# Kernel tuning notes

Hardware: AMD Instinct MI355X
Metric: run time of the kernel (lower is better)

## Reference

```python
import jax, jax.numpy as jnp
import numpy as np

N_PRO, N_WAT, E = 60000, 40000, 1000000
N = N_PRO + N_WAT
IN_DIM, HID, HEADS = 21, 32, 4
EDGE_K, EDGE_DIM = 32, 32
RADIUS_MAX = 5.0
FF_HID, OUT_DIM = 128, 2
HC = HID * HEADS


def setup_inputs() -> dict:
    key = jax.random.key(0)
    ks = jax.random.split(key, 32)

    def glorot(k, shape):
        fan = shape[0] + shape[-1]
        return jax.random.normal(k, shape, jnp.float32) * jnp.sqrt(2.0 / fan)

    inp = {
        'protein_pos': jax.random.normal(ks[0], (N_PRO, 3), jnp.float32),
        'water_pos': jax.random.normal(ks[1], (N_WAT, 3), jnp.float32),
        'protein_features': jax.random.uniform(ks[2], (N_PRO, IN_DIM), jnp.float32),
        'edge_index': jax.random.randint(ks[3], (2, E), 0, N, jnp.int64),
        'gamma': jnp.array([10.0], jnp.float32),
        # feature_emb
        'Wf': glorot(ks[4], (IN_DIM, HID)), 'bf': jnp.zeros((HID,), jnp.float32),
        # edge_emb
        'We': glorot(ks[5], (EDGE_K, EDGE_DIM)), 'be': jnp.zeros((EDGE_DIM,), jnp.float32),
        # conv1 (in: HID)
        'W1': glorot(ks[6], (HID, HC)),
        'att_src1': glorot(ks[7], (HEADS, HID)), 'att_dst1': glorot(ks[8], (HEADS, HID)),
        'Wedge1': glorot(ks[9], (EDGE_DIM, HC)), 'att_edge1': glorot(ks[10], (HEADS, HID)),
        'b1': jnp.zeros((HC,), jnp.float32),
        # conv2 (in: HC)
        'W2': glorot(ks[11], (HC, HC)),
        'att_src2': glorot(ks[12], (HEADS, HID)), 'att_dst2': glorot(ks[13], (HEADS, HID)),
        'Wedge2': glorot(ks[14], (EDGE_DIM, HC)), 'att_edge2': glorot(ks[15], (HEADS, HID)),
        'b2': jnp.zeros((HC,), jnp.float32),
        # mlp
        'Wm1': glorot(ks[16], (HC, FF_HID)), 'bm1': jnp.zeros((FF_HID,), jnp.float32),
        'Wm2': glorot(ks[17], (FF_HID, OUT_DIM)), 'bm2': jnp.zeros((OUT_DIM,), jnp.float32),
    }
    return inp


def gat_conv(h, edge_attr, src, dst, W, att_s, att_d, Wedge, att_e, b):
    # h: [N, Din] -> x: [N, H, C]; edge features only modulate attention logits.
    x = (h @ W).reshape(N, HEADS, HID)
    e = (edge_attr @ Wedge).reshape(-1, HEADS, HID)
    a_s = jnp.einsum('nhc,hc->nh', x, att_s)   # [N,H]
    a_d = jnp.einsum('nhc,hc->nh', x, att_d)   # [N,H]
    a_e = jnp.einsum('ehc,hc->eh', e, att_e)   # [E,H]
    alpha = jax.nn.leaky_relu(a_s[src] + a_d[dst] + a_e, 0.2)  # [E,H]
    # segment softmax over incoming edges of each dst node
    m = jax.ops.segment_max(alpha, dst, num_segments=N)
    m = jnp.where(jnp.isfinite(m), m, 0.0)
    ex = jnp.exp(alpha - m[dst])
    den = jax.ops.segment_sum(ex, dst, num_segments=N)
    coef = ex / (den[dst] + 1e-16)             # [E,H]
    msg = x[src] * coef[:, :, None]            # [E,H,C]
    out = jax.ops.segment_sum(msg, dst, num_segments=N)  # [N,H,C]
    return out.reshape(N, HC) + b


def reference(protein_pos, water_pos, protein_features, edge_index, gamma,
              Wf, bf, We, be,
              W1, att_src1, att_dst1, Wedge1, att_edge1, b1,
              W2, att_src2, att_dst2, Wedge2, att_edge2, b2,
              Wm1, bm1, Wm2, bm2):
    pos = jnp.concatenate([protein_pos, water_pos], axis=0)  # [N,3]
    src, dst = edge_index[0], edge_index[1]
    edge_vec = pos[dst] - pos[src]
    edge_dis = jnp.linalg.norm(edge_vec, axis=-1)            # [E]
    # RBF expansion of distances
    centers = jnp.linspace(0.0, RADIUS_MAX, EDGE_K)
    edge_h = jnp.exp(-gamma[0] * (edge_dis[:, None] - centers[None, :]) ** 2)  # [E,K]
    edge_attr = edge_h @ We + be                             # [E,EDGE_DIM]

    # water nodes get one-hot 'water' feature in last slot
    water_feat = jnp.zeros((N_WAT, IN_DIM), protein_features.dtype).at[:, -1].set(1.0)
    feats = jnp.concatenate([protein_features, water_feat], axis=0)
    h = feats @ Wf + bf                                      # [N,HID]

    h = jax.nn.elu(gat_conv(h, edge_attr, src, dst, W1, att_src1, att_dst1, Wedge1, att_edge1, b1))
    h = jax.nn.elu(gat_conv(h, edge_attr, src, dst, W2, att_src2, att_dst2, Wedge2, att_edge2, b2))

    h = jax.nn.relu(h @ Wm1 + bm1) @ Wm2 + bm2               # [N,OUT_DIM]
    return h[N_PRO:]                                         # water nodes only
```

## Files before the change

kernel.cpp:

```cpp
#include <hip/hip_runtime.h>
#include <hip/hip_fp16.h>
#include <stdint.h>

#define N_PRO 60000
#define N_WAT 40000
#define NN    100000
#define NNP   100032
#define NE    1000000
#define IN_DIM 21
#define HID    32
#define HEADS  4
#define HC     128
#define EDGE_K 32
#define LUTN   2048
#define NH0B  ((NNP * 32) / 256)
#define NBUCK 196
#define EPT   8
#define SCATB ((NE / EPT + 255) / 256)
#define FCAP  6144

typedef _Float16 half8 __attribute__((ext_vector_type(8)));
typedef float    f32x4 __attribute__((ext_vector_type(4)));

__global__ __launch_bounds__(256) void k_small(
    const float* We, const float* be,
    const float* Wedge1, const float* atte1,
    const float* Wedge2, const float* atte2,
    const float* Wf, const float* bfv,
    const float* W1, const float* atts1, const float* attd1,
    float* smallw)
{
    __shared__ float V[2][128];
    int t = threadIdx.x;
    {
        int l = t >> 7, dh = t & 127, d = dh >> 2, h = dh & 3;
        const float* Wg = l ? Wedge2 : Wedge1;
        const float* ae = l ? atte2 : atte1;
        float s = 0.f;
        for (int c = 0; c < HID; c++)
            s += Wg[d * HC + h * HID + c] * ae[h * HID + c];
        V[l][dh] = s;
    }
    __syncthreads();
    {
        int l = t >> 7, kh = t & 127, k = kh >> 2, h = kh & 3;
        float s = 0.f;
        for (int d = 0; d < 32; d++)
            s += We[k * 32 + d] * V[l][d * 4 + h];
        smallw[(l ? 132 : 0) + kh] = s;
    }
    if (t < 8) {
        int l = t >> 2, h = t & 3;
        float s = 0.f;
        for (int d = 0; d < 32; d++)
            s += be[d] * V[l][d * 4 + h];
        smallw[(l ? 260 : 128) + h] = s;
    }
    if (t >= 32 && t < 64) {
        int c = t - 32;
        smallw[264 + c] = Wf[20 * 32 + c] + bfv[c];
    }
    {
        int side = t >> 7;
        int h = (t >> 5) & 3, c = t & 31;
        const float* av = side ? attd1 : atts1;
        float s = 0.f;
        for (int j = 0; j < 32; j++)
            s += W1[c * 128 + h * 32 + j] * av[h * 32 + j];
        smallw[(side ? 424 : 296) + (t & 127)] = s;
    }
}

__global__ __launch_bounds__(256) void k_lut(
    const float* __restrict__ smallw, const float* __restrict__ gamma,
    float* __restrict__ lut)
{
    int e = blockIdx.x * 256 + threadIdx.x;
    if (e >= 2 * LUTN) return;
    int layer = e >> 11, bin = e & (LUTN - 1);
    const float* U = smallw + (layer ? 132 : 0);
    const float* aeb = smallw + (layer ? 260 : 128);
    float dd = bin * (1.0f / 256.0f);
    float g = gamma[0];
    float a0 = aeb[0], a1 = aeb[1], a2 = aeb[2], a3 = aeb[3];
    const float step = 5.0f / 31.0f;
    #pragma unroll
    for (int k = 0; k < EDGE_K; k++) {
        float tt = dd - (float)k * step;
        float r = __expf(-g * tt * tt);
        a0 += r * U[k * 4 + 0];
        a1 += r * U[k * 4 + 1];
        a2 += r * U[k * 4 + 2];
        a3 += r * U[k * 4 + 3];
    }
    *(float4*)&lut[(size_t)e * 4] = make_float4(a0, a1, a2, a3);
}

__global__ __launch_bounds__(256) void k_h0(
    const float* __restrict__ pf, const float* __restrict__ Wf,
    const float* __restrict__ bfv, const float* __restrict__ smallw,
    __half* __restrict__ h0, float* __restrict__ asd)
{
    int t = threadIdx.x;
    __shared__ float Wfs[IN_DIM * 32];
    __shared__ float bfs[32];
    __shared__ float h0w[32];
    __shared__ float vas[128], vad[128];
    for (int i = t; i < IN_DIM * 32; i += 256) Wfs[i] = Wf[i];
    if (t < 32) { bfs[t] = bfv[t]; h0w[t] = smallw[264 + t]; }
    if (t < 128) vas[t] = smallw[296 + t];
    else         vad[t - 128] = smallw[424 + (t - 128)];
    __syncthreads();
    int id = blockIdx.x * 256 + t;
    int n = id >> 5, c = id & 31;
    if (n >= NNP) return;
    float v;
    if (n < N_PRO) {
        float s = bfs[c];
        for (int k = 0; k < IN_DIM; k++)
            s += pf[n * IN_DIM + k] * Wfs[k * 32 + c];
        v = s;
    } else {
        v = h0w[c];
    }
    h0[(size_t)n * 32 + c] = __float2half(v);
    float ps[4], pd[4];
    #pragma unroll
    for (int h = 0; h < 4; h++) {
        ps[h] = v * vas[h * 32 + c];
        pd[h] = v * vad[h * 32 + c];
    }
    #pragma unroll
    for (int m = 1; m < 32; m <<= 1) {
        #pragma unroll
        for (int h = 0; h < 4; h++) {
            ps[h] += __shfl_xor(ps[h], m, 64);
            pd[h] += __shfl_xor(pd[h], m, 64);
        }
    }
    if ((t & 31) == 0) {
        *(float4*)&asd[(size_t)n * 8]     = make_float4(ps[0], ps[1], ps[2], ps[3]);
        *(float4*)&asd[(size_t)n * 8 + 4] = make_float4(pd[0], pd[1], pd[2], pd[3]);
    }
}

__global__ __launch_bounds__(256) void k_bcnt(
    const int* __restrict__ ei, int* __restrict__ gbh)
{
    __shared__ int lh[256];
    int t = threadIdx.x;
    lh[t] = 0;
    __syncthreads();
    int e0 = (blockIdx.x * 256 + t) * EPT;
    if (e0 < NE) {
        int4 da = *(const int4*)&ei[NE + e0];
        int4 db = *(const int4*)&ei[NE + e0 + 4];
        int ds[8] = {da.x, da.y, da.z, da.w, db.x, db.y, db.z, db.w};
        #pragma unroll
        for (int j = 0; j < EPT; j++)
            if ((unsigned)ds[j] < (unsigned)NN)
                atomicAdd(&lh[ds[j] >> 9], 1);
    }
    __syncthreads();
    if (t < NBUCK && lh[t]) atomicAdd(&gbh[t], lh[t]);
}

__global__ __launch_bounds__(256) void k_bscan(
    const int* __restrict__ gbh, int* __restrict__ gboff,
    int* __restrict__ gcur, int* __restrict__ offp)
{
    __shared__ int s[256];
    int t = threadIdx.x;
    int v = (t < NBUCK) ? gbh[t] : 0;
    s[t] = v;
    __syncthreads();
    #pragma unroll
    for (int o = 1; o < 256; o <<= 1) {
        int x = (t >= o) ? s[t - o] : 0;
        __syncthreads();
        s[t] += x;
        __syncthreads();
    }
    int ex = s[t] - v;
    if (t < NBUCK) { gboff[t] = ex; gcur[t] = ex; }
    if (t == NBUCK - 1) { gboff[NBUCK] = s[t]; offp[NN] = s[t]; }
}

__global__ __launch_bounds__(256) void k_scat(
    const int* __restrict__ ei, const float* __restrict__ ppos,
    const float* __restrict__ wpos, int* __restrict__ gcur,
    uint2* __restrict__ ebuf2)
{
    __shared__ int lh[256];
    __shared__ int lbase[256];
    int t = threadIdx.x;
    lh[t] = 0;
    __syncthreads();
    int e0 = (blockIdx.x * 256 + t) * EPT;
    int bkt[EPT], rnk[EPT];
    unsigned rec0[EPT], rec1[EPT];
    #pragma unroll
    for (int j = 0; j < EPT; j++) bkt[j] = -1;
    if (e0 < NE) {
        int4 sa = *(const int4*)&ei[e0];
        int4 sb = *(const int4*)&ei[e0 + 4];
        int4 da = *(const int4*)&ei[NE + e0];
        int4 db = *(const int4*)&ei[NE + e0 + 4];
        int ss[8] = {sa.x, sa.y, sa.z, sa.w, sb.x, sb.y, sb.z, sb.w};
        int ds[8] = {da.x, da.y, da.z, da.w, db.x, db.y, db.z, db.w};
        #pragma unroll
        for (int j = 0; j < EPT; j++) {
            int s = ss[j], d = ds[j];
            if ((unsigned)d < (unsigned)NN) {
                const float* ps = (s < N_PRO) ? &ppos[s * 3] : &wpos[(s - N_PRO) * 3];
                const float* pd = (d < N_PRO) ? &ppos[d * 3] : &wpos[(d - N_PRO) * 3];
                float dx = pd[0] - ps[0];
                float dy = pd[1] - ps[1];
                float dz = pd[2] - ps[2];
                float dist = sqrtf(dx * dx + dy * dy + dz * dz);
                unsigned code = (unsigned)fminf(dist * 4096.0f, 32767.0f);
                bkt[j] = d >> 9;
                rec0[j] = ((unsigned)d << 15) | code;
                rec1[j] = (unsigned)s;
                rnk[j] = atomicAdd(&lh[bkt[j]], 1);
            }
        }
    }
    __syncthreads();
    if (t < NBUCK) lbase[t] = lh[t] ? atomicAdd(&gcur[t], lh[t]) : 0;
    __syncthreads();
    #pragma unroll
    for (int j = 0; j < EPT; j++)
        if (bkt[j] >= 0)
            ebuf2[lbase[bkt[j]] + rnk[j]] = make_uint2(rec0[j], rec1[j]);
}

__global__ __launch_bounds__(1024) void k_fine(
    const int* __restrict__ gboff, const uint2* __restrict__ ebuf2,
    const float* __restrict__ lutg, const float* __restrict__ asd,
    int* __restrict__ offp, unsigned* __restrict__ e4,
    float* __restrict__ wb)
{
    __shared__ uint2 eL[FCAP];
    __shared__ int lcnt[512], lexc[512], ssc[512];
    int b = blockIdx.x, t = threadIdx.x;
    int beg = gboff[b];
    int nb = gboff[b + 1] - beg;
    bool inl = (nb <= FCAP);
    if (inl)
        for (int i = t; i < nb; i += 1024) eL[i] = ebuf2[beg + i];
    if (t < 512) lcnt[t] = 0;
    __syncthreads();
    for (int i = t; i < nb; i += 1024) {
        uint2 u = inl ? eL[i] : ebuf2[beg + i];
        atomicAdd(&lcnt[(u.x >> 15) & 511], 1);
    }
    __syncthreads();
    int c = (t < 512) ? lcnt[t] : 0;
    if (t < 512) ssc[t] = c;
    __syncthreads();
    for (int o = 1; o < 512; o <<= 1) {
        int x = (t >= o && t < 512) ? ssc[t - o] : 0;
        __syncthreads();
        if (t < 512) ssc[t] += x;
        __syncthreads();
    }
    if (t < 512) {
        lexc[t] = ssc[t] - c;
        int node = b * 512 + t;
        if (node < NN) offp[node] = beg + lexc[t];
        lcnt[t] = 0;
    }
    __syncthreads();
    for (int i = t; i < nb; i += 1024) {
        uint2 u = inl ? eL[i] : ebuf2[beg + i];
        int ln = (int)((u.x >> 15) & 511u);
        int r = atomicAdd(&lcnt[ln], 1);
        int p = beg + lexc[ln] + r;
        unsigned code = u.x & 32767u;
        unsigned s = u.y;
        e4[p] = (s << 15) | code;
        int n = (b << 9) + ln;
        float f = fminf((float)code * 0.0625f, (float)(LUTN - 2));
        int i0 = (int)f;
        float fr = f - (float)i0;
        float4 A = *(const float4*)&lutg[(size_t)i0 * 4];
        float4 B = *(const float4*)&lutg[(size_t)(i0 + 1) * 4];
        float4 as4 = *(const float4*)&asd[(size_t)s * 8];
        float4 ad4 = *(const float4*)&asd[(size_t)n * 8 + 4];
        float v0 = as4.x + ad4.x + A.x + (B.x - A.x) * fr;
        float v1 = as4.y + ad4.y + A.y + (B.y - A.y) * fr;
        float v2 = as4.z + ad4.z + A.z + (B.z - A.z) * fr;
        float v3 = as4.w + ad4.w + A.w + (B.w - A.w) * fr;
        v0 = fmaxf(v0, 0.2f * v0);
        v1 = fmaxf(v1, 0.2f * v1);
        v2 = fmaxf(v2, 0.2f * v2);
        v3 = fmaxf(v3, 0.2f * v3);
        *(float4*)&wb[(size_t)p * 4] = make_float4(
            __expf(v0), __expf(v1), __expf(v2), __expf(v3));
    }
}

__global__ __launch_bounds__(256) void k_xm(
    const __half* __restrict__ h, const float* __restrict__ Wg,
    const float* __restrict__ atts, const float* __restrict__ attd,
    __half* __restrict__ x16, float* __restrict__ asd)
{
    __shared__ __half Wt[128 * 136];
    __shared__ float attS[128], attD[128];
    int t = threadIdx.x;
    for (int i = t; i < 128 * 32; i += 256) {
        int c = i & 127, d = (i >> 7) * 4;
        float w0 = Wg[(d + 0) * 128 + c];
        float w1 = Wg[(d + 1) * 128 + c];
        float w2 = Wg[(d + 2) * 128 + c];
        float w3 = Wg[(d + 3) * 128 + c];
        __half2 p0 = __floats2half2_rn(w0, w1);
        __half2 p1 = __floats2half2_rn(w2, w3);
        uint2 pk;
        pk.x = *(unsigned*)&p0;
        pk.y = *(unsigned*)&p1;
        *(uint2*)&Wt[c * 136 + d] = pk;
    }
    if (t < 128) { attS[t] = atts[t]; attD[t] = attd[t]; }
    __syncthreads();
    int wv = t >> 6, lane = t & 63;
    int m16 = lane & 15, quad = lane >> 4;
    int n0 = blockIdx.x * 64 + wv * 16;
    f32x4 acc[8];
    #pragma unroll
    for (int ct = 0; ct < 8; ct++) acc[ct] = (f32x4){0.f, 0.f, 0.f, 0.f};
    #pragma unroll
    for (int ks = 0; ks < 4; ks++) {
        int d0 = ks * 32 + quad * 8;
        half8 bf = *(const half8*)&h[(size_t)(n0 + m16) * 128 + d0];
        #pragma unroll
        for (int ct = 0; ct < 8; ct++) {
            half8 af = *(const half8*)&Wt[(ct * 16 + m16) * 136 + d0];
            acc[ct] = __builtin_amdgcn_mfma_f32_16x16x32_f16(af, bf, acc[ct], 0, 0, 0);
        }
    }
    __half* xrow = &x16[(size_t)(n0 + m16) * 128 + quad * 4];
    float ps[4] = {0.f, 0.f, 0.f, 0.f}, pd[4] = {0.f, 0.f, 0.f, 0.f};
    #pragma unroll
    for (int ct = 0; ct < 8; ct++) {
        f32x4 a = acc[ct];
        __half2 h0p = __floats2half2_rn(a[0], a[1]);
        __half2 h1p = __floats2half2_rn(a[2], a[3]);
        uint2 pk;
        pk.x = *(unsigned*)&h0p;
        pk.y = *(unsigned*)&h1p;
        *(uint2*)&xrow[ct * 16] = pk;
        int cb = ct * 16 + quad * 4;
        int hh = ct >> 1;
        ps[hh] += a[0] * attS[cb] + a[1] * attS[cb + 1]
                + a[2] * attS[cb + 2] + a[3] * attS[cb + 3];
        pd[hh] += a[0] * attD[cb] + a[1] * attD[cb + 1]
                + a[2] * attD[cb + 2] + a[3] * attD[cb + 3];
    }
    #pragma unroll
    for (int hh = 0; hh < 4; hh++) {
        ps[hh] += __shfl_xor(ps[hh], 16, 64);
        ps[hh] += __shfl_xor(ps[hh], 32, 64);
        pd[hh] += __shfl_xor(pd[hh], 16, 64);
        pd[hh] += __shfl_xor(pd[hh], 32, 64);
    }
    if (lane < 16) {
        int n = n0 + m16;
        *(float4*)&asd[(size_t)n * 8]     = make_float4(ps[0], ps[1], ps[2], ps[3]);
        *(float4*)&asd[(size_t)n * 8 + 4] = make_float4(pd[0], pd[1], pd[2], pd[3]);
    }
}

__global__ __launch_bounds__(256) void k_w2(
    const int* __restrict__ off, const unsigned* __restrict__ e4,
    const float* __restrict__ lutg, const float* __restrict__ asd,
    float* __restrict__ wb)
{
    int wv = threadIdx.x >> 6, lane = threadIdx.x & 63;
    int n = N_PRO + blockIdx.x * 4 + wv;
    if (n >= NN) return;
    int beg = off[n], end = off[n + 1];
    float4 ad4 = *(const float4*)&asd[(size_t)n * 8 + 4];
    for (int i = beg + lane; i < end; i += 64) {
        unsigned u = e4[i];
        unsigned s = u >> 15;
        float f = fminf((float)(u & 32767u) * 0.0625f, (float)(LUTN - 2));
        int i0 = (int)f;
        float fr = f - (float)i0;
        float4 A = *(const float4*)&lutg[(size_t)i0 * 4];
        float4 B = *(const float4*)&lutg[(size_t)(i0 + 1) * 4];
        float4 as4 = *(const float4*)&asd[(size_t)s * 8];
        float v0 = as4.x + ad4.x + A.x + (B.x - A.x) * fr;
        float v1 = as4.y + ad4.y + A.y + (B.y - A.y) * fr;
        float v2 = as4.z + ad4.z + A.z + (B.z - A.z) * fr;
        float v3 = as4.w + ad4.w + A.w + (B.w - A.w) * fr;
        v0 = fmaxf(v0, 0.2f * v0);
        v1 = fmaxf(v1, 0.2f * v1);
        v2 = fmaxf(v2, 0.2f * v2);
        v3 = fmaxf(v3, 0.2f * v3);
        *(float4*)&wb[(size_t)i * 4] = make_float4(
            __expf(v0), __expf(v1), __expf(v2), __expf(v3));
    }
}

__global__ __launch_bounds__(256) void k_aggz(
    const int* __restrict__ off, const unsigned* __restrict__ e4,
    const float* __restrict__ wb, const __half* __restrict__ h016,
    __half* __restrict__ zbuf)
{
    int t = threadIdx.x;
    int wv = t >> 6, lane = t & 63;
    int g = lane >> 4, q = lane & 15;
    int n = blockIdx.x * 16 + wv * 4 + g;
    int beg = off[n], end = off[n + 1];
    const __half2* x2 = (const __half2*)h016;
    float a0x = 0.f, a0y = 0.f, a1x = 0.f, a1y = 0.f;
    float a2x = 0.f, a2y = 0.f, a3x = 0.f, a3y = 0.f;
    float l0 = 0.f, l1 = 0.f, l2 = 0.f, l3 = 0.f;
    int i = beg;
    for (; i + 1 < end; i += 2) {
        unsigned u0 = e4[i], u1 = e4[i + 1];
        float4 w0 = *(const float4*)&wb[(size_t)i * 4];
        float4 w1 = *(const float4*)&wb[(size_t)(i + 1) * 4];
        float2 x0 = __half22float2(x2[(u0 >> 15) * 16u + q]);
        float2 x1 = __half22float2(x2[(u1 >> 15) * 16u + q]);
        a0x += w0.x * x0.x + w1.x * x1.x;  a0y += w0.x * x0.y + w1.x * x1.y;
        a1x += w0.y * x0.x + w1.y * x1.x;  a1y += w0.y * x0.y + w1.y * x1.y;
        a2x += w0.z * x0.x + w1.z * x1.x;  a2y += w0.z * x0.y + w1.z * x1.y;
        a3x += w0.w * x0.x + w1.w * x1.x;  a3y += w0.w * x0.y + w1.w * x1.y;
        l0 += w0.x + w1.x;  l1 += w0.y + w1.y;
        l2 += w0.z + w1.z;  l3 += w0.w + w1.w;
    }
    if (i < end) {
        unsigned u0 = e4[i];
        float4 w0 = *(const float4*)&wb[(size_t)i * 4];
        float2 x0 = __half22float2(x2[(u0 >> 15) * 16u + q]);
        a0x += w0.x * x0.x;  a0y += w0.x * x0.y;
        a1x += w0.y * x0.x;  a1y += w0.y * x0.y;
        a2x += w0.z * x0.x;  a2y += w0.z * x0.y;
        a3x += w0.w * x0.x;  a3y += w0.w * x0.y;
        l0 += w0.x; l1 += w0.y; l2 += w0.z; l3 += w0.w;
    }
    float i0v = 1.0f / (l0 + 1e-16f);
    float i1v = 1.0f / (l1 + 1e-16f);
    float i2v = 1.0f / (l2 + 1e-16f);
    float i3v = 1.0f / (l3 + 1e-16f);
    __half* zr = &zbuf[(size_t)n * 128];
    *(__half2*)&zr[      q * 2] = __floats2half2_rn(a0x * i0v, a0y * i0v);
    *(__half2*)&zr[32  + q * 2] = __floats2half2_rn(a1x * i1v, a1y * i1v);
    *(__half2*)&zr[64  + q * 2] = __floats2half2_rn(a2x * i2v, a2y * i2v);
    *(__half2*)&zr[96  + q * 2] = __floats2half2_rn(a3x * i3v, a3y * i3v);
}

__global__ __launch_bounds__(256) void k_zm(
    const __half* __restrict__ zbuf, const float* __restrict__ W1g,
    const float* __restrict__ b1, __half* __restrict__ hbuf)
{
    __shared__ __half Wt[128 * 40];
    int t = threadIdx.x;
    for (int i = t; i < 128 * 8; i += 256) {
        int c = i & 127, k4 = (i >> 7) * 4;
        float w0 = W1g[(k4 + 0) * 128 + c];
        float w1 = W1g[(k4 + 1) * 128 + c];
        float w2 = W1g[(k4 + 2) * 128 + c];
        float w3 = W1g[(k4 + 3) * 128 + c];
        __half2 p0 = __floats2half2_rn(w0, w1);
        __half2 p1 = __floats2half2_rn(w2, w3);
        uint2 pk;
        pk.x = *(unsigned*)&p0;
        pk.y = *(unsigned*)&p1;
        *(uint2*)&Wt[c * 40 + k4] = pk;
    }
    __syncthreads();
    int wv = t >> 6, lane = t & 63;
    int m16 = lane & 15, quad = lane >> 4;
    int n0 = blockIdx.x * 64 + wv * 16;
    half8 bf[4];
    #pragma unroll
    for (int hh = 0; hh < 4; hh++)
        bf[hh] = *(const half8*)&zbuf[(size_t)(n0 + m16) * 128 + hh * 32 + quad * 8];
    f32x4 acc[8];
    #pragma unroll
    for (int ct = 0; ct < 8; ct++) {
        half8 af = *(const half8*)&Wt[(ct * 16 + m16) * 40 + quad * 8];
        acc[ct] = __builtin_amdgcn_mfma_f32_16x16x32_f16(
            af, bf[ct >> 1], (f32x4){0.f, 0.f, 0.f, 0.f}, 0, 0, 0);
    }
    __half* orow = &hbuf[(size_t)(n0 + m16) * 128 + quad * 4];
    #pragma unroll
    for (int ct = 0; ct < 8; ct++) {
        int cb = ct * 16 + quad * 4;
        float4 bb = *(const float4*)&b1[cb];
        float r0 = acc[ct][0] + bb.x;
        float r1 = acc[ct][1] + bb.y;
        float r2 = acc[ct][2] + bb.z;
        float r3 = acc[ct][3] + bb.w;
        r0 = r0 > 0.f ? r0 : __expf(r0) - 1.0f;
        r1 = r1 > 0.f ? r1 : __expf(r1) - 1.0f;
        r2 = r2 > 0.f ? r2 : __expf(r2) - 1.0f;
        r3 = r3 > 0.f ? r3 : __expf(r3) - 1.0f;
        __half2 ha = __floats2half2_rn(r0, r1);
        __half2 hb = __floats2half2_rn(r2, r3);
        uint2 pk;
        pk.x = *(unsigned*)&ha;
        pk.y = *(unsigned*)&hb;
        *(uint2*)&orow[ct * 16] = pk;
    }
}

__global__ __launch_bounds__(256) void k_agg2(
    const int* __restrict__ off, const unsigned* __restrict__ e4,
    const float* __restrict__ wb, const __half* __restrict__ x16,
    const float* __restrict__ bias, __half* __restrict__ hout)
{
    int t = threadIdx.x;
    int wv = t >> 6, lane = t & 63;
    int g = lane >> 5, q = lane & 31;
    int n = N_PRO + blockIdx.x * 8 + wv * 2 + g;
    int h = q >> 3;
    int beg = off[n], end = off[n + 1];
    float ax = 0.f, ay = 0.f, az = 0.f, aw = 0.f, ls = 0.f;
    int i = beg;
    for (; i + 1 < end; i += 2) {
        unsigned u0 = e4[i], u1 = e4[i + 1];
        float w0 = wb[(size_t)i * 4 + h];
        float w1 = wb[(size_t)(i + 1) * 4 + h];
        float2 r0 = *(const float2*)&x16[(size_t)(u0 >> 15) * 128 + q * 4];
        float2 r1 = *(const float2*)&x16[(size_t)(u1 >> 15) * 128 + q * 4];
        float2 f00 = __half22float2(*(__half2*)&r0.x);
        float2 f01 = __half22float2(*(__half2*)&r0.y);
        float2 f10 = __half22float2(*(__half2*)&r1.x);
        float2 f11 = __half22float2(*(__half2*)&r1.y);
        ax += w0 * f00.x + w1 * f10.x;
        ay += w0 * f00.y + w1 * f10.y;
        az += w0 * f01.x + w1 * f11.x;
        aw += w0 * f01.y + w1 * f11.y;
        ls += w0 + w1;
    }
    if (i < end) {
        unsigned u0 = e4[i];
        float w0 = wb[(size_t)i * 4 + h];
        float2 r0 = *(const float2*)&x16[(size_t)(u0 >> 15) * 128 + q * 4];
        float2 f00 = __half22float2(*(__half2*)&r0.x);
        float2 f01 = __half22float2(*(__half2*)&r0.y);
        ax += w0 * f00.x; ay += w0 * f00.y;
        az += w0 * f01.x; aw += w0 * f01.y;
        ls += w0;
    }
    float inv = 1.0f / (ls + 1e-16f);
    float4 bb = *(const float4*)&bias[q * 4];
    float o0 = ax * inv + bb.x;
    float o1 = ay * inv + bb.y;
    float o2 = az * inv + bb.z;
    float o3 = aw * inv + bb.w;
    o0 = o0 > 0.f ? o0 : __expf(o0) - 1.0f;
    o1 = o1 > 0.f ? o1 : __expf(o1) - 1.0f;
    o2 = o2 > 0.f ? o2 : __expf(o2) - 1.0f;
    o3 = o3 > 0.f ? o3 : __expf(o3) - 1.0f;
    __half2 ha = __floats2half2_rn(o0, o1);
    __half2 hb = __floats2half2_rn(o2, o3);
    uint2 pk;
    pk.x = *(unsigned*)&ha;
    pk.y = *(unsigned*)&hb;
    *(uint2*)&hout[(size_t)n * 128 + q * 4] = pk;
}

__global__ __launch_bounds__(256) void k_mlp(
    const __half* __restrict__ hh, const float* __restrict__ Wm1,
    const float* __restrict__ bm1, const float* __restrict__ Wm2,
    const float* __restrict__ bm2, float* __restrict__ out)
{
    __shared__ __half Wt[128 * 136];
    __shared__ float b1s[128];
    __shared__ float w2s[256];
    int t = threadIdx.x;
    for (int i = t; i < 128 * 32; i += 256) {
        int c = i & 127, d = (i >> 7) * 4;
        float w0 = Wm1[(d + 0) * 128 + c];
        float w1 = Wm1[(d + 1) * 128 + c];
        float w2 = Wm1[(d + 2) * 128 + c];
        float w3 = Wm1[(d + 3) * 128 + c];
        __half2 p0 = __floats2half2_rn(w0, w1);
        __half2 p1 = __floats2half2_rn(w2, w3);
        uint2 pk;
        pk.x = *(unsigned*)&p0;
        pk.y = *(unsigned*)&p1;
        *(uint2*)&Wt[c * 136 + d] = pk;
    }
    if (t < 128) b1s[t] = bm1[t];
    w2s[t] = Wm2[t];
    __syncthreads();
    int wv = t >> 6, lane = t & 63;
    int m16 = lane & 15, quad = lane >> 4;
    int n0 = blockIdx.x * 64 + wv * 16;
    f32x4 acc[8];
    #pragma unroll
    for (int ct = 0; ct < 8; ct++) acc[ct] = (f32x4){0.f, 0.f, 0.f, 0.f};
    #pragma unroll
    for (int ks = 0; ks < 4; ks++) {
        int d0 = ks * 32 + quad * 8;
        half8 bf = *(const half8*)&hh[(size_t)(N_PRO + n0 + m16) * 128 + d0];
        #pragma unroll
        for (int ct = 0; ct < 8; ct++) {
            half8 af = *(const half8*)&Wt[(ct * 16 + m16) * 136 + d0];
            acc[ct] = __builtin_amdgcn_mfma_f32_16x16x32_f16(af, bf, acc[ct], 0, 0, 0);
        }
    }
    float p0 = 0.f, p1 = 0.f;
    #pragma unroll
    for (int ct = 0; ct < 8; ct++) {
        int cb = ct * 16 + quad * 4;
        float4 bb = *(const float4*)&b1s[cb];
        float r0 = fmaxf(acc[ct][0] + bb.x, 0.f);
        float r1 = fmaxf(acc[ct][1] + bb.y, 0.f);
        float r2 = fmaxf(acc[ct][2] + bb.z, 0.f);
        float r3 = fmaxf(acc[ct][3] + bb.w, 0.f);
        p0 += r0 * w2s[(cb + 0) * 2] + r1 * w2s[(cb + 1) * 2]
            + r2 * w2s[(cb + 2) * 2] + r3 * w2s[(cb + 3) * 2];
        p1 += r0 * w2s[(cb + 0) * 2 + 1] + r1 * w2s[(cb + 1) * 2 + 1]
            + r2 * w2s[(cb + 2) * 2 + 1] + r3 * w2s[(cb + 3) * 2 + 1];
    }
    p0 += __shfl_xor(p0, 16, 64);
    p0 += __shfl_xor(p0, 32, 64);
    p1 += __shfl_xor(p1, 16, 64);
    p1 += __shfl_xor(p1, 32, 64);
    if (lane < 16) {
        int wn = n0 + m16;
        *(float2*)&out[(size_t)wn * 2] = make_float2(p0 + bm2[0], p1 + bm2[1]);
    }
}

extern "C" void kernel_launch(void* const* d_in, const int* in_sizes, int n_in,
                              void* d_out, int out_size, void* d_ws, size_t ws_size,
                              hipStream_t stream)
{
    const float* ppos   = (const float*)d_in[0];
    const float* wpos   = (const float*)d_in[1];
    const float* pfeat  = (const float*)d_in[2];
    const int*   ei     = (const int*)d_in[3];
    const float* gamma  = (const float*)d_in[4];
    const float* Wf     = (const float*)d_in[5];
    const float* bfv    = (const float*)d_in[6];
    const float* We     = (const float*)d_in[7];
    const float* be     = (const float*)d_in[8];
    const float* W1     = (const float*)d_in[9];
    const float* atts1  = (const float*)d_in[10];
    const float* attd1  = (const float*)d_in[11];
    const float* Wedge1 = (const float*)d_in[12];
    const float* atte1  = (const float*)d_in[13];
    const float* b1     = (const float*)d_in[14];
    const float* W2     = (const float*)d_in[15];
    const float* atts2  = (const float*)d_in[16];
    const float* attd2  = (const float*)d_in[17];
    const float* Wedge2 = (const float*)d_in[18];
    const float* atte2  = (const float*)d_in[19];
    const float* b2     = (const float*)d_in[20];
    const float* Wm1    = (const float*)d_in[21];
    const float* bm1    = (const float*)d_in[22];
    const float* Wm2    = (const float*)d_in[23];
    const float* bm2    = (const float*)d_in[24];
    float* out = (float*)d_out;

    char* ws = (char*)d_ws;
    size_t o = 0;
    auto alloc = [&](size_t bytes) -> char* {
        char* p = ws + o;
        o += (bytes + 255) & ~(size_t)255;
        return p;
    };
    __half*   h0      = (__half*)alloc((size_t)NNP * 32 * 2);
    __half*   x16     = (__half*)alloc((size_t)NNP * 128 * 2);
    __half*   hbuf    = (__half*)alloc((size_t)NNP * 128 * 2);
    float*    asd     = (float*)alloc((size_t)NNP * 8 * 4);
    float*    wb      = (float*)alloc((size_t)NE * 4 * 4);
    int*      offp    = (int*)alloc((size_t)(NN + 1) * 4);
    unsigned* e4      = (unsigned*)alloc((size_t)NE * 4);
    int*      gbh     = (int*)alloc(256 * 4);
    int*      gboff   = (int*)alloc(256 * 4);
    int*      gcur    = (int*)alloc(256 * 4);
    float*    smallw  = (float*)alloc(4096);
    float*    lutbuf  = (float*)alloc((size_t)2 * LUTN * 4 * 4);
    uint2*    ebuf2   = (uint2*)hbuf;

    hipMemsetAsync(gbh, 0, 256 * 4, stream);
    k_small<<<1, 256, 0, stream>>>(We, be, Wedge1, atte1, Wedge2, atte2, Wf, bfv,
                                   W1, atts1, attd1, smallw);
    k_lut<<<(2 * LUTN + 255) / 256, 256, 0, stream>>>(smallw, gamma, lutbuf);
    k_h0<<<NH0B, 256, 0, stream>>>(pfeat, Wf, bfv, smallw, h0, asd);
    k_bcnt<<<SCATB, 256, 0, stream>>>(ei, gbh);
    k_bscan<<<1, 256, 0, stream>>>(gbh, gboff, gcur, offp);
    k_scat<<<SCATB, 256, 0, stream>>>(ei, ppos, wpos, gcur, ebuf2);
    k_fine<<<NBUCK, 1024, 0, stream>>>(gboff, ebuf2, lutbuf, asd, offp, e4, wb);
    k_aggz<<<NN / 16, 256, 0, stream>>>(offp, e4, wb, h0, x16);
    k_zm<<<NNP / 64, 256, 0, stream>>>(x16, W1, b1, hbuf);
    k_xm<<<NNP / 64, 256, 0, stream>>>(hbuf, W2, atts2, attd2, x16, asd);
    k_w2<<<N_WAT / 4, 256, 0, stream>>>(offp, e4, lutbuf + (size_t)LUTN * 4, asd, wb);
    k_agg2<<<N_WAT / 8, 256, 0, stream>>>(offp, e4, wb, x16, b2, hbuf);
    k_mlp<<<N_WAT / 64, 256, 0, stream>>>(hbuf, Wm1, bm1, Wm2, bm2, out);
}
```

Measured before the change: 325.3 us.

## Fuse bucket count into h0, fuse conv2 weights into aggregation, faster scans

Merges the bucket-histogram kernel into k_h0 as extra blocks, so one launch covers both and they can run concurrently. Removes k_w2 and computes the conv2 attention weights inline in k_agg2 from the LUT and asd, which drops the write and reread of wb. Replaces the shared-memory Hillis-Steele scan in k_fine with a wave-level shuffle scan plus a small cross-wave scan, and unrolls the k_aggz edge loop by 4 for more memory-level parallelism. In exchange, k_agg2 recomputes each edge weight in every one of the 8 lanes that share a head, and the merged k_h0 now has two divergent block types.

After: 310.5 us. -4.6%, faster.

```diff
diff --git a/kernel.cpp b/kernel.cpp
--- a/kernel.cpp
+++ b/kernel.cpp
@@ -99,9 +99,28 @@
 __global__ __launch_bounds__(256) void k_h0(
     const float* __restrict__ pf, const float* __restrict__ Wf,
     const float* __restrict__ bfv, const float* __restrict__ smallw,
+    const int* __restrict__ ei, int* __restrict__ gbh,
     __half* __restrict__ h0, float* __restrict__ asd)
 {
     int t = threadIdx.x;
+    if (blockIdx.x >= NH0B) {
+        __shared__ int lh[256];
+        lh[t] = 0;
+        __syncthreads();
+        int e0 = ((blockIdx.x - NH0B) * 256 + t) * EPT;
+        if (e0 < NE) {
+            int4 da = *(const int4*)&ei[NE + e0];
+            int4 db = *(const int4*)&ei[NE + e0 + 4];
+            int ds[8] = {da.x, da.y, da.z, da.w, db.x, db.y, db.z, db.w};
+            #pragma unroll
+            for (int j = 0; j < EPT; j++)
+                if ((unsigned)ds[j] < (unsigned)NN)
+                    atomicAdd(&lh[ds[j] >> 9], 1);
+        }
+        __syncthreads();
+        if (t < NBUCK && lh[t]) atomicAdd(&gbh[t], lh[t]);
+        return;
+    }
     __shared__ float Wfs[IN_DIM * 32];
     __shared__ float bfs[32];
     __shared__ float h0w[32];
@@ -142,27 +161,6 @@
         *(float4*)&asd[(size_t)n * 8]     = make_float4(ps[0], ps[1], ps[2], ps[3]);
         *(float4*)&asd[(size_t)n * 8 + 4] = make_float4(pd[0], pd[1], pd[2], pd[3]);
     }
-}
-
-__global__ __launch_bounds__(256) void k_bcnt(
-    const int* __restrict__ ei, int* __restrict__ gbh)
-{
-    __shared__ int lh[256];
-    int t = threadIdx.x;
-    lh[t] = 0;
-    __syncthreads();
-    int e0 = (blockIdx.x * 256 + t) * EPT;
-    if (e0 < NE) {
-        int4 da = *(const int4*)&ei[NE + e0];
-        int4 db = *(const int4*)&ei[NE + e0 + 4];
-        int ds[8] = {da.x, da.y, da.z, da.w, db.x, db.y, db.z, db.w};
-        #pragma unroll
-        for (int j = 0; j < EPT; j++)
-            if ((unsigned)ds[j] < (unsigned)NN)
-                atomicAdd(&lh[ds[j] >> 9], 1);
-    }
-    __syncthreads();
-    if (t < NBUCK && lh[t]) atomicAdd(&gbh[t], lh[t]);
 }
 
 __global__ __launch_bounds__(256) void k_bscan(
@@ -242,7 +240,8 @@
     float* __restrict__ wb)
 {
     __shared__ uint2 eL[FCAP];
-    __shared__ int lcnt[512], lexc[512], ssc[512];
+    __shared__ int lcnt[512], lexc[512];
+    __shared__ int wsum[8];
     int b = blockIdx.x, t = threadIdx.x;
     int beg = gboff[b];
     int nb = gboff[b + 1] - beg;
@@ -256,17 +255,32 @@
         atomicAdd(&lcnt[(u.x >> 15) & 511], 1);
     }
     __syncthreads();
-    int c = (t < 512) ? lcnt[t] : 0;
-    if (t < 512) ssc[t] = c;
-    __syncthreads();
-    for (int o = 1; o < 512; o <<= 1) {
-        int x = (t >= o && t < 512) ? ssc[t - o] : 0;
-        __syncthreads();
-        if (t < 512) ssc[t] += x;
-        __syncthreads();
-    }
     if (t < 512) {
-        lexc[t] = ssc[t] - c;
+        int c = lcnt[t];
+        int lane = t & 63;
+        int v = c;
+        #pragma unroll
+        for (int d = 1; d < 64; d <<= 1) {
+            int x = __shfl_up(v, d, 64);
+            if (lane >= d) v += x;
+        }
+        if (lane == 63) wsum[t >> 6] = v;
+        lexc[t] = v - c;
+    }
+    __syncthreads();
+    if (t < 8) {
+        int orig = wsum[t];
+        int v = orig;
+        #pragma unroll
+        for (int d = 1; d < 8; d <<= 1) {
+            int x = __shfl_up(v, d, 64);
+            if (t >= d) v += x;
+        }
+        wsum[t] = v - orig;
+    }
+    __syncthreads();
+    if (t < 512) {
+        lexc[t] += wsum[t >> 6];
         int node = b * 512 + t;
         if (node < NN) offp[node] = beg + lexc[t];
         lcnt[t] = 0;
@@ -372,38 +386,6 @@
     }
 }
 
-__global__ __launch_bounds__(256) void k_w2(
-    const int* __restrict__ off, const unsigned* __restrict__ e4,
-    const float* __restrict__ lutg, const float* __restrict__ asd,
-    float* __restrict__ wb)
-{
-    int wv = threadIdx.x >> 6, lane = threadIdx.x & 63;
-    int n = N_PRO + blockIdx.x * 4 + wv;
-    if (n >= NN) return;
-    int beg = off[n], end = off[n + 1];
-    float4 ad4 = *(const float4*)&asd[(size_t)n * 8 + 4];
-    for (int i = beg + lane; i < end; i += 64) {
-        unsigned u = e4[i];
-        unsigned s = u >> 15;
-        float f = fminf((float)(u & 32767u) * 0.0625f, (float)(LUTN - 2));
-        int i0 = (int)f;
-        float fr = f - (float)i0;
-        float4 A = *(const float4*)&lutg[(size_t)i0 * 4];
-        float4 B = *(const float4*)&lutg[(size_t)(i0 + 1) * 4];
-        float4 as4 = *(const float4*)&asd[(size_t)s * 8];
-        float v0 = as4.x + ad4.x + A.x + (B.x - A.x) * fr;
-        float v1 = as4.y + ad4.y + A.y + (B.y - A.y) * fr;
-        float v2 = as4.z + ad4.z + A.z + (B.z - A.z) * fr;
-        float v3 = as4.w + ad4.w + A.w + (B.w - A.w) * fr;
-        v0 = fmaxf(v0, 0.2f * v0);
-        v1 = fmaxf(v1, 0.2f * v1);
-        v2 = fmaxf(v2, 0.2f * v2);
-        v3 = fmaxf(v3, 0.2f * v3);
-        *(float4*)&wb[(size_t)i * 4] = make_float4(
-            __expf(v0), __expf(v1), __expf(v2), __expf(v3));
-    }
-}
-
 __global__ __launch_bounds__(256) void k_aggz(
     const int* __restrict__ off, const unsigned* __restrict__ e4,
     const float* __restrict__ wb, const __half* __restrict__ h016,
@@ -419,20 +401,31 @@
     float a2x = 0.f, a2y = 0.f, a3x = 0.f, a3y = 0.f;
     float l0 = 0.f, l1 = 0.f, l2 = 0.f, l3 = 0.f;
     int i = beg;
-    for (; i + 1 < end; i += 2) {
-        unsigned u0 = e4[i], u1 = e4[i + 1];
+    for (; i + 3 < end; i += 4) {
+        unsigned u0 = e4[i],     u1 = e4[i + 1];
+        unsigned u2 = e4[i + 2], u3 = e4[i + 3];
         float4 w0 = *(const float4*)&wb[(size_t)i * 4];
         float4 w1 = *(const float4*)&wb[(size_t)(i + 1) * 4];
+        float4 w2 = *(const float4*)&wb[(size_t)(i + 2) * 4];
+        float4 w3 = *(const float4*)&wb[(size_t)(i + 3) * 4];
         float2 x0 = __half22float2(x2[(u0 >> 15) * 16u + q]);
         float2 x1 = __half22float2(x2[(u1 >> 15) * 16u + q]);
-        a0x += w0.x * x0.x + w1.x * x1.x;  a0y += w0.x * x0.y + w1.x * x1.y;
-        a1x += w0.y * x0.x + w1.y * x1.x;  a1y += w0.y * x0.y + w1.y * x1.y;
-        a2x += w0.z * x0.x + w1.z * x1.x;  a2y += w0.z * x0.y + w1.z * x1.y;
-        a3x += w0.w * x0.x + w1.w * x1.x;  a3y += w0.w * x0.y + w1.w * x1.y;
-        l0 += w0.x + w1.x;  l1 += w0.y + w1.y;
-        l2 += w0.z + w1.z;  l3 += w0.w + w1.w;
-    }
-    if (i < end) {
+        float2 x2v = __half22float2(x2[(u2 >> 15) * 16u + q]);
+        float2 x3 = __half22float2(x2[(u3 >> 15) * 16u + q]);
+        a0x += w0.x * x0.x + w1.x * x1.x + w2.x * x2v.x + w3.x * x3.x;
+        a0y += w0.x * x0.y + w1.x * x1.y + w2.x * x2v.y + w3.x * x3.y;
+        a1x += w0.y * x0.x + w1.y * x1.x + w2.y * x2v.x + w3.y * x3.x;
+        a1y += w0.y * x0.y + w1.y * x1.y + w2.y * x2v.y + w3.y * x3.y;
+        a2x += w0.z * x0.x + w1.z * x1.x + w2.z * x2v.x + w3.z * x3.x;
+        a2y += w0.z * x0.y + w1.z * x1.y + w2.z * x2v.y + w3.z * x3.y;
+        a3x += w0.w * x0.x + w1.w * x1.x + w2.w * x2v.x + w3.w * x3.x;
+        a3y += w0.w * x0.y + w1.w * x1.y + w2.w * x2v.y + w3.w * x3.y;
+        l0 += (w0.x + w1.x) + (w2.x + w3.x);
+        l1 += (w0.y + w1.y) + (w2.y + w3.y);
+        l2 += (w0.z + w1.z) + (w2.z + w3.z);
+        l3 += (w0.w + w1.w) + (w2.w + w3.w);
+    }
+    for (; i < end; i++) {
         unsigned u0 = e4[i];
         float4 w0 = *(const float4*)&wb[(size_t)i * 4];
         float2 x0 = __half22float2(x2[(u0 >> 15) * 16u + q]);
@@ -511,8 +504,9 @@
 
 __global__ __launch_bounds__(256) void k_agg2(
     const int* __restrict__ off, const unsigned* __restrict__ e4,
-    const float* __restrict__ wb, const __half* __restrict__ x16,
-    const float* __restrict__ bias, __half* __restrict__ hout)
+    const float* __restrict__ lutg, const float* __restrict__ asd,
+    const __half* __restrict__ x16, const float* __restrict__ bias,
+    __half* __restrict__ hout)
 {
     int t = threadIdx.x;
     int wv = t >> 6, lane = t & 63;
@@ -520,14 +514,26 @@
     int n = N_PRO + blockIdx.x * 8 + wv * 2 + g;
     int h = q >> 3;
     int beg = off[n], end = off[n + 1];
+    float adh = asd[(size_t)n * 8 + 4 + h];
     float ax = 0.f, ay = 0.f, az = 0.f, aw = 0.f, ls = 0.f;
     int i = beg;
     for (; i + 1 < end; i += 2) {
         unsigned u0 = e4[i], u1 = e4[i + 1];
-        float w0 = wb[(size_t)i * 4 + h];
-        float w1 = wb[(size_t)(i + 1) * 4 + h];
-        float2 r0 = *(const float2*)&x16[(size_t)(u0 >> 15) * 128 + q * 4];
-        float2 r1 = *(const float2*)&x16[(size_t)(u1 >> 15) * 128 + q * 4];
+        unsigned s0 = u0 >> 15, s1 = u1 >> 15;
+        float f0 = fminf((float)(u0 & 32767u) * 0.0625f, (float)(LUTN - 2));
+        float f1 = fminf((float)(u1 & 32767u) * 0.0625f, (float)(LUTN - 2));
+        int i00 = (int)f0, i10 = (int)f1;
+        float fr0 = f0 - (float)i00, fr1 = f1 - (float)i10;
+        float A0 = lutg[i00 * 4 + h], B0 = lutg[(i00 + 1) * 4 + h];
+        float A1 = lutg[i10 * 4 + h], B1 = lutg[(i10 + 1) * 4 + h];
+        float as0 = asd[(size_t)s0 * 8 + h], as1 = asd[(size_t)s1 * 8 + h];
+        float2 r0 = *(const float2*)&x16[(size_t)s0 * 128 + q * 4];
+        float2 r1 = *(const float2*)&x16[(size_t)s1 * 128 + q * 4];
+        float v0 = as0 + adh + A0 + (B0 - A0) * fr0;
+        float v1 = as1 + adh + A1 + (B1 - A1) * fr1;
+        v0 = fmaxf(v0, 0.2f * v0);
+        v1 = fmaxf(v1, 0.2f * v1);
+        float w0 = __expf(v0), w1 = __expf(v1);
         float2 f00 = __half22float2(*(__half2*)&r0.x);
         float2 f01 = __half22float2(*(__half2*)&r0.y);
         float2 f10 = __half22float2(*(__half2*)&r1.x);
@@ -540,8 +546,16 @@
     }
     if (i < end) {
         unsigned u0 = e4[i];
-        float w0 = wb[(size_t)i * 4 + h];
-        float2 r0 = *(const float2*)&x16[(size_t)(u0 >> 15) * 128 + q * 4];
+        unsigned s0 = u0 >> 15;
+        float f0 = fminf((float)(u0 & 32767u) * 0.0625f, (float)(LUTN - 2));
+        int i00 = (int)f0;
+        float fr0 = f0 - (float)i00;
+        float A0 = lutg[i00 * 4 + h], B0 = lutg[(i00 + 1) * 4 + h];
+        float as0 = asd[(size_t)s0 * 8 + h];
+        float2 r0 = *(const float2*)&x16[(size_t)s0 * 128 + q * 4];
+        float v0 = as0 + adh + A0 + (B0 - A0) * fr0;
+        v0 = fmaxf(v0, 0.2f * v0);
+        float w0 = __expf(v0);
         float2 f00 = __half22float2(*(__half2*)&r0.x);
         float2 f01 = __half22float2(*(__half2*)&r0.y);
         ax += w0 * f00.x; ay += w0 * f00.y;
@@ -687,15 +701,13 @@
     k_small<<<1, 256, 0, stream>>>(We, be, Wedge1, atte1, Wedge2, atte2, Wf, bfv,
                                    W1, atts1, attd1, smallw);
     k_lut<<<(2 * LUTN + 255) / 256, 256, 0, stream>>>(smallw, gamma, lutbuf);
-    k_h0<<<NH0B, 256, 0, stream>>>(pfeat, Wf, bfv, smallw, h0, asd);
-    k_bcnt<<<SCATB, 256, 0, stream>>>(ei, gbh);
+    k_h0<<<NH0B + SCATB, 256, 0, stream>>>(pfeat, Wf, bfv, smallw, ei, gbh, h0, asd);
     k_bscan<<<1, 256, 0, stream>>>(gbh, gboff, gcur, offp);
     k_scat<<<SCATB, 256, 0, stream>>>(ei, ppos, wpos, gcur, ebuf2);
     k_fine<<<NBUCK, 1024, 0, stream>>>(gboff, ebuf2, lutbuf, asd, offp, e4, wb);
     k_aggz<<<NN / 16, 256, 0, stream>>>(offp, e4, wb, h0, x16);
     k_zm<<<NNP / 64, 256, 0, stream>>>(x16, W1, b1, hbuf);
     k_xm<<<NNP / 64, 256, 0, stream>>>(hbuf, W2, atts2, attd2, x16, asd);
-    k_w2<<<N_WAT / 4, 256, 0, stream>>>(offp, e4, lutbuf + (size_t)LUTN * 4, asd, wb);
-    k_agg2<<<N_WAT / 8, 256, 0, stream>>>(offp, e4, wb, x16, b2, hbuf);
+    k_agg2<<<N_WAT / 8, 256, 0, stream>>>(offp, e4, lutbuf + (size_t)LUTN * 4, asd, x16, b2, hbuf);
     k_mlp<<<N_WAT / 64, 256, 0, stream>>>(hbuf, Wm1, bm1, Wm2, bm2, out);
 }
```
